# Performance work log

Hardware: AMD Instinct MI355X
Metric: run time of the kernel (lower is better)

Reference implementation:

```python
import jax, jax.numpy as jnp
import numpy as np

N = 100000      # n_nodes
E = 1600000     # n_edges (avg degree 16)
IN, HID, OUT = 128, 128, 64
P = 0.5         # dropout prob


def setup_inputs() -> dict:
    key = jax.random.key(0)
    k = jax.random.split(key, 6)
    x = jax.random.normal(k[0], (N, IN), dtype=jnp.float32)
    edge_index = jax.random.randint(k[1], (2, E), 0, N, dtype=jnp.int32)
    W1 = jax.random.normal(k[2], (IN, HID), dtype=jnp.float32) / np.sqrt(IN)
    b1 = jnp.zeros((HID,), dtype=jnp.float32)
    W2 = jax.random.normal(k[3], (HID, OUT), dtype=jnp.float32) / np.sqrt(HID)
    b2 = jnp.zeros((OUT,), dtype=jnp.float32)
    return {"x": x, "edge_index": edge_index, "W1": W1, "b1": b1, "W2": W2, "b2": b2}


def gcn_conv(x, W, b, src, dst, num_nodes):
    """PyG GCNConv: add self-loops, symmetric D^-1/2 A D^-1/2 normalization,
    linear transform then scatter-add aggregation at destination nodes."""
    loop = jnp.arange(num_nodes, dtype=src.dtype)
    s = jnp.concatenate([src, loop])  # [E+N]
    d = jnp.concatenate([dst, loop])
    deg = jax.ops.segment_sum(jnp.ones_like(d, dtype=x.dtype), d, num_segments=num_nodes)
    dinv = jnp.where(deg > 0, jax.lax.rsqrt(jnp.maximum(deg, 1e-12)), 0.0)
    norm = dinv[s] * dinv[d]                     # [E+N]
    h = x @ W                                    # [N, F_out] (transform first: cheaper)
    msg = h[s] * norm[:, None]                   # gather + scale
    out = jax.ops.segment_sum(msg, d, num_segments=num_nodes)  # scatter-add
    return out + b


def reference(x, edge_index, W1, b1, W2, b2):
    src, dst = edge_index[0], edge_index[1]
    h = jax.nn.relu(gcn_conv(x, W1, b1, src, dst, N))
    # F.dropout(training=True) with a fixed key for determinism
    keep = jax.random.bernoulli(jax.random.key(42), 1.0 - P, h.shape)
    h = jnp.where(keep, h / (1.0 - P), 0.0)
    return gcn_conv(h, W2, b2, src, dst, N)
```

## Files before the change

### kernel.cpp

```cpp
#include <hip/hip_runtime.h>


constexpr int NN    = 100000;
constexpr int NE    = 1600000;
constexpr int SCAN_CHUNK = 2048;
constexpr int NSCAN = (NN + SCAN_CHUNK - 1) / SCAN_CHUNK;

typedef __attribute__((ext_vector_type(8))) short short8v;
typedef __attribute__((ext_vector_type(4))) float f32x4;

__device__ __forceinline__ float bf2f(unsigned short u) {
  return __uint_as_float(((unsigned)u) << 16);
}
__device__ __forceinline__ unsigned short f2bf(float f) {
  unsigned x = __float_as_uint(f);
  return (unsigned short)((x + 0x7fffu + ((x >> 16) & 1u)) >> 16);
}
__device__ __forceinline__ float lo16(unsigned p) { return bf2f((unsigned short)(p & 0xffffu)); }
__device__ __forceinline__ float hi16(unsigned p) { return bf2f((unsigned short)(p >> 16)); }

__device__ __forceinline__ unsigned tf_rotl(unsigned x, int r) {
  return (x << r) | (x >> (32 - r));
}

__device__ __forceinline__ void threefry2x32_0_42(unsigned in0, unsigned in1,
                                                  unsigned& o0, unsigned& o1) {
  const unsigned K0 = 0u, K1 = 42u;
  const unsigned K2 = 0x1BD11BDAu ^ K0 ^ K1;
  unsigned x0 = in0 + K0, x1 = in1 + K1;
#define TFR(r) { x0 += x1; x1 = tf_rotl(x1, r); x1 ^= x0; }
  TFR(13) TFR(15) TFR(26) TFR(6)
  x0 += K1; x1 += K2 + 1u;
  TFR(17) TFR(29) TFR(16) TFR(24)
  x0 += K2; x1 += K0 + 2u;
  TFR(13) TFR(15) TFR(26) TFR(6)
  x0 += K0; x1 += K1 + 3u;
  TFR(17) TFR(29) TFR(16) TFR(24)
  x0 += K1; x1 += K2 + 4u;
  TFR(13) TFR(15) TFR(26) TFR(6)
  x0 += K2; x1 += K0 + 5u;
#undef TFR
  o0 = x0; o1 = x1;
}

__device__ __forceinline__ bool dropout_keep(unsigned i) {
  unsigned a, b; threefry2x32_0_42(0u, i, a, b);
  return ((a ^ b) >> 31) == 0u;
}


__global__ __launch_bounds__(256) void hist_kernel(const int* __restrict__ dst,
                                                   int* __restrict__ cnt) {
  int e = blockIdx.x * 256 + threadIdx.x;
  if (e < NE) atomicAdd(&cnt[dst[e]], 1);
}

__global__ __launch_bounds__(256) void scan1_kernel(const int* __restrict__ cnt,
                                                    int* __restrict__ off,
                                                    int* __restrict__ blksum,
                                                    float* __restrict__ dinv) {
  __shared__ int tsum[256];
  const int base = blockIdx.x * SCAN_CHUNK + threadIdx.x * 8;
  int v[8]; int s = 0;
#pragma unroll
  for (int j = 0; j < 8; j++) {
    int idx = base + j;
    v[j] = (idx < NN) ? cnt[idx] : 0;
    s += v[j];
    if (idx < NN) dinv[idx] = rsqrtf((float)v[j] + 1.0f);
  }
  tsum[threadIdx.x] = s;
  __syncthreads();
  for (int d = 1; d < 256; d <<= 1) {
    int t = (threadIdx.x >= d) ? tsum[threadIdx.x - d] : 0;
    __syncthreads();
    tsum[threadIdx.x] += t;
    __syncthreads();
  }
  int run = tsum[threadIdx.x] - s;
  if (threadIdx.x == 255) blksum[blockIdx.x] = tsum[255];
#pragma unroll
  for (int j = 0; j < 8; j++) {
    int idx = base + j;
    if (idx < NN) { off[idx] = run; run += v[j]; }
  }
}

__global__ void scan2_kernel(int* __restrict__ blksum, int* __restrict__ off) {
  if (threadIdx.x == 0) {
    int run = 0;
    for (int i = 0; i < NSCAN; i++) { int t = blksum[i]; blksum[i] = run; run += t; }
    off[NN] = NE;
  }
}

__global__ __launch_bounds__(256) void scan3_kernel(int* __restrict__ off,
                                                    const int* __restrict__ blksum) {
  const int base = blockIdx.x * SCAN_CHUNK + threadIdx.x * 8;
  const int add = blksum[blockIdx.x];
#pragma unroll
  for (int j = 0; j < 8; j++) {
    int idx = base + j;
    if (idx < NN) off[idx] += add;
  }
}

__global__ __launch_bounds__(256) void permute_kernel(const int* __restrict__ src,
                                                      const int* __restrict__ dst,
                                                      int* __restrict__ cur,
                                                      int* __restrict__ srcs) {
  int e = blockIdx.x * 256 + threadIdx.x;
  if (e >= NE) return;
  int p = atomicAdd(&cur[dst[e]], 1);
  srcs[p] = src[e];
}


template <int C, bool BF16_IN>
__global__ __launch_bounds__(256) void gemm_mfma_kernel(const void* __restrict__ Xv,
                                                        const float* __restrict__ W,
                                                        unsigned short* __restrict__ H,
                                                        int nrows) {
  constexpr int STR = 136;
  __shared__ unsigned short Xs[64 * STR];
  __shared__ unsigned short Wt[C * STR];
  const int row0 = blockIdx.x * 64;
  const int nr = min(64, nrows - row0);
  const int tid = threadIdx.x;

  for (int t = tid; t < C * 64; t += 256) {
    int n = t % C, kk = t / C;
    unsigned pk = ((unsigned)f2bf(W[(2 * kk + 1) * C + n]) << 16) | f2bf(W[(2 * kk) * C + n]);
    *(unsigned*)&Wt[n * STR + 2 * kk] = pk;
  }
  if (BF16_IN) {
    const unsigned* X = (const unsigned*)Xv + (size_t)row0 * 64;
    for (int t = tid; t < 64 * 64; t += 256) {
      int r = t >> 6, kp = t & 63;
      unsigned p = (r < nr) ? X[r * 64 + kp] : 0u;
      *(unsigned*)&Xs[r * STR + 2 * kp] = p;
    }
  } else {
    const float* X = (const float*)Xv + (size_t)row0 * 128;
    for (int t = tid; t < 64 * 64; t += 256) {
      int r = t >> 6, kp = t & 63;
      unsigned p = 0u;
      if (r < nr) {
        float2 v = *(const float2*)&X[r * 128 + 2 * kp];
        p = ((unsigned)f2bf(v.y) << 16) | f2bf(v.x);
      }
      *(unsigned*)&Xs[r * STR + 2 * kp] = p;
    }
  }
  __syncthreads();

  const int w  = tid >> 6;
  const int l  = tid & 63;
  const int lr = l & 15;
  const int lk = l >> 4;
  constexpr int NT = C / 16;

  f32x4 acc[NT];
#pragma unroll
  for (int nt = 0; nt < NT; nt++) acc[nt] = (f32x4){0.f, 0.f, 0.f, 0.f};

  short8v afr[4];
  const int arow = w * 16 + lr;
#pragma unroll
  for (int ks = 0; ks < 4; ks++)
    afr[ks] = *(const short8v*)&Xs[arow * STR + ks * 32 + lk * 8];

#pragma unroll
  for (int nt = 0; nt < NT; nt++) {
    const int ncol = nt * 16 + lr;
#pragma unroll
    for (int ks = 0; ks < 4; ks++) {
      short8v bfr = *(const short8v*)&Wt[ncol * STR + ks * 32 + lk * 8];
      acc[nt] = __builtin_amdgcn_mfma_f32_16x16x32_bf16(afr[ks], bfr, acc[nt], 0, 0, 0);
    }
  }

#pragma unroll
  for (int nt = 0; nt < NT; nt++) {
#pragma unroll
    for (int r = 0; r < 4; r++) {
      int row = w * 16 + lk * 4 + r;
      if (row < nr) H[(size_t)(row0 + row) * C + nt * 16 + lr] = f2bf(acc[nt][r]);
    }
  }
}


__global__ __launch_bounds__(256) void gather1_kernel(const int* __restrict__ off,
                                                      const int* __restrict__ srcs,
                                                      const unsigned* __restrict__ hb,
                                                      const float* __restrict__ dinv,
                                                      const float* __restrict__ b1,
                                                      unsigned* __restrict__ hd) {
  int nid = blockIdx.x * 4 + (threadIdx.x >> 6);
  if (nid >= NN) return;
  int c = threadIdx.x & 63;
  float di = dinv[nid];
  unsigned hp = hb[(size_t)nid * 64 + c];
  float a0 = lo16(hp) * di * di;
  float a1 = hi16(hp) * di * di;
  int beg = off[nid], end = off[nid + 1];
  int e = beg;
  for (; e + 8 <= end; e += 8) {
    int s[8]; float w[8]; unsigned p[8];
#pragma unroll
    for (int j = 0; j < 8; j++) s[j] = srcs[e + j];
#pragma unroll
    for (int j = 0; j < 8; j++) w[j] = dinv[s[j]] * di;
#pragma unroll
    for (int j = 0; j < 8; j++) p[j] = hb[(size_t)s[j] * 64 + c];
#pragma unroll
    for (int j = 0; j < 8; j++) {
      a0 = fmaf(lo16(p[j]), w[j], a0);
      a1 = fmaf(hi16(p[j]), w[j], a1);
    }
  }
  for (; e < end; e++) {
    int s = srcs[e];
    float w = dinv[s] * di;
    unsigned p = hb[(size_t)s * 64 + c];
    a0 = fmaf(lo16(p), w, a0);
    a1 = fmaf(hi16(p), w, a1);
  }
  a0 += b1[2 * c];
  a1 += b1[2 * c + 1];
  a0 = fmaxf(a0, 0.f);
  a1 = fmaxf(a1, 0.f);
  unsigned i0 = (unsigned)nid * 128u + 2u * (unsigned)c;
  a0 = dropout_keep(i0)      ? 2.f * a0 : 0.f;
  a1 = dropout_keep(i0 + 1u) ? 2.f * a1 : 0.f;
  hd[(size_t)nid * 64 + c] = ((unsigned)f2bf(a1) << 16) | f2bf(a0);
}


__global__ __launch_bounds__(256) void gather2_kernel(const int* __restrict__ off,
                                                      const int* __restrict__ srcs,
                                                      const unsigned short* __restrict__ h2b,
                                                      const float* __restrict__ dinv,
                                                      const float* __restrict__ b2,
                                                      float* __restrict__ out) {
  int nid = blockIdx.x * 4 + (threadIdx.x >> 6);
  if (nid >= NN) return;
  int c = threadIdx.x & 63;
  float di = dinv[nid];
  float acc = bf2f(h2b[(size_t)nid * 64 + c]) * di * di;
  int beg = off[nid], end = off[nid + 1];
  int e = beg;
  for (; e + 8 <= end; e += 8) {
    int s[8]; float w[8]; float v[8];
#pragma unroll
    for (int j = 0; j < 8; j++) s[j] = srcs[e + j];
#pragma unroll
    for (int j = 0; j < 8; j++) w[j] = dinv[s[j]] * di;
#pragma unroll
    for (int j = 0; j < 8; j++) v[j] = bf2f(h2b[(size_t)s[j] * 64 + c]);
#pragma unroll
    for (int j = 0; j < 8; j++) acc = fmaf(v[j], w[j], acc);
  }
  for (; e < end; e++) {
    int s = srcs[e];
    acc = fmaf(bf2f(h2b[(size_t)s * 64 + c]), dinv[s] * di, acc);
  }
  out[(size_t)nid * 64 + c] = acc + b2[c];
}


extern "C" void kernel_launch(void* const* d_in, const int* in_sizes, int n_in,
                              void* d_out, int out_size, void* d_ws, size_t ws_size,
                              hipStream_t stream) {
  const float* x  = (const float*)d_in[0];
  const int*   ei = (const int*)d_in[1];
  const float* W1 = (const float*)d_in[2];
  const float* b1 = (const float*)d_in[3];
  const float* W2 = (const float*)d_in[4];
  const float* b2 = (const float*)d_in[5];
  float* out = (float*)d_out;

  const int* src = ei;
  const int* dst = ei + NE;

  char* p = (char*)d_ws;
  auto take = [&](size_t bytes) { char* q = p; p += (bytes + 15) & ~size_t(15); return q; };
  int*      cnt    = (int*)take(sizeof(int) * NN);
  int*      cur    = (int*)take(sizeof(int) * NN);
  int*      off    = (int*)take(sizeof(int) * (NN + 1));
  int*      blksum = (int*)take(sizeof(int) * NSCAN);
  float*    dinv   = (float*)take(sizeof(float) * NN);
  int*      srcs   = (int*)take(sizeof(int) * NE);
  unsigned* hb     = (unsigned*)take(sizeof(unsigned) * (size_t)NN * 64);
  unsigned* hd     = (unsigned*)take(sizeof(unsigned) * (size_t)NN * 64);
  unsigned* h2b    = (unsigned*)take(sizeof(unsigned) * (size_t)NN * 32);

  hipMemsetAsync(cnt, 0, sizeof(int) * NN, stream);
  hist_kernel<<<(NE + 255) / 256, 256, 0, stream>>>(dst, cnt);
  scan1_kernel<<<NSCAN, 256, 0, stream>>>(cnt, off, blksum, dinv);
  scan2_kernel<<<1, 64, 0, stream>>>(blksum, off);
  scan3_kernel<<<NSCAN, 256, 0, stream>>>(off, blksum);
  hipMemcpyAsync(cur, off, sizeof(int) * NN, hipMemcpyDeviceToDevice, stream);
  permute_kernel<<<(NE + 255) / 256, 256, 0, stream>>>(src, dst, cur, srcs);

  gemm_mfma_kernel<128, false><<<(NN + 63) / 64, 256, 0, stream>>>(
      x, W1, (unsigned short*)hb, NN);
  gather1_kernel<<<(NN + 3) / 4, 256, 0, stream>>>(off, srcs, hb, dinv, b1, hd);

  gemm_mfma_kernel<64, true><<<(NN + 63) / 64, 256, 0, stream>>>(
      hd, W2, (unsigned short*)h2b, NN);
  gather2_kernel<<<(NN + 3) / 4, 256, 0, stream>>>(
      off, srcs, (const unsigned short*)h2b, dinv, b2, out);
}
```

Baseline: 513.9 us.

## Build CSR with two-level bucket sort instead of per-node atomics

```diff
diff --git a/kernel.cpp b/kernel.cpp
--- a/kernel.cpp
+++ b/kernel.cpp
@@ -1,10 +1,9 @@
 #include <hip/hip_runtime.h>
 
 
-constexpr int NN    = 100000;
-constexpr int NE    = 1600000;
-constexpr int SCAN_CHUNK = 2048;
-constexpr int NSCAN = (NN + SCAN_CHUNK - 1) / SCAN_CHUNK;
+constexpr int NN = 100000;
+constexpr int NE = 1600000;
+constexpr int NB = (NN + 127) / 128;
 
 typedef __attribute__((ext_vector_type(8))) short short8v;
 typedef __attribute__((ext_vector_type(4))) float f32x4;
@@ -49,70 +48,91 @@
 }
 
 
-__global__ __launch_bounds__(256) void hist_kernel(const int* __restrict__ dst,
-                                                   int* __restrict__ cnt) {
-  int e = blockIdx.x * 256 + threadIdx.x;
-  if (e < NE) atomicAdd(&cnt[dst[e]], 1);
-}
-
-__global__ __launch_bounds__(256) void scan1_kernel(const int* __restrict__ cnt,
-                                                    int* __restrict__ off,
-                                                    int* __restrict__ blksum,
-                                                    float* __restrict__ dinv) {
-  __shared__ int tsum[256];
-  const int base = blockIdx.x * SCAN_CHUNK + threadIdx.x * 8;
-  int v[8]; int s = 0;
-#pragma unroll
-  for (int j = 0; j < 8; j++) {
-    int idx = base + j;
-    v[j] = (idx < NN) ? cnt[idx] : 0;
-    s += v[j];
-    if (idx < NN) dinv[idx] = rsqrtf((float)v[j] + 1.0f);
-  }
-  tsum[threadIdx.x] = s;
-  __syncthreads();
-  for (int d = 1; d < 256; d <<= 1) {
-    int t = (threadIdx.x >= d) ? tsum[threadIdx.x - d] : 0;
+__global__ __launch_bounds__(256) void histB_kernel(const int* __restrict__ dst,
+                                                    int* __restrict__ bcnt) {
+  __shared__ int h[NB];
+  for (int i = threadIdx.x; i < NB; i += 256) h[i] = 0;
+  __syncthreads();
+  for (int e = blockIdx.x * 256 + threadIdx.x; e < NE; e += gridDim.x * 256)
+    atomicAdd(&h[dst[e] >> 7], 1);
+  __syncthreads();
+  for (int i = threadIdx.x; i < NB; i += 256)
+    if (h[i]) atomicAdd(&bcnt[i], h[i]);
+}
+
+__global__ __launch_bounds__(1024) void scanB_kernel(const int* __restrict__ bcnt,
+                                                     int* __restrict__ bbase,
+                                                     int* __restrict__ bcur,
+                                                     int* __restrict__ off) {
+  __shared__ int s[1024];
+  int t = threadIdx.x;
+  s[t] = (t < NB) ? bcnt[t] : 0;
+  __syncthreads();
+  for (int d = 1; d < 1024; d <<= 1) {
+    int v = (t >= d) ? s[t - d] : 0;
     __syncthreads();
-    tsum[threadIdx.x] += t;
+    s[t] += v;
     __syncthreads();
   }
-  int run = tsum[threadIdx.x] - s;
-  if (threadIdx.x == 255) blksum[blockIdx.x] = tsum[255];
-#pragma unroll
-  for (int j = 0; j < 8; j++) {
-    int idx = base + j;
-    if (idx < NN) { off[idx] = run; run += v[j]; }
-  }
-}
-
-__global__ void scan2_kernel(int* __restrict__ blksum, int* __restrict__ off) {
-  if (threadIdx.x == 0) {
-    int run = 0;
-    for (int i = 0; i < NSCAN; i++) { int t = blksum[i]; blksum[i] = run; run += t; }
-    off[NN] = NE;
-  }
-}
-
-__global__ __launch_bounds__(256) void scan3_kernel(int* __restrict__ off,
-                                                    const int* __restrict__ blksum) {
-  const int base = blockIdx.x * SCAN_CHUNK + threadIdx.x * 8;
-  const int add = blksum[blockIdx.x];
-#pragma unroll
-  for (int j = 0; j < 8; j++) {
-    int idx = base + j;
-    if (idx < NN) off[idx] += add;
-  }
-}
-
-__global__ __launch_bounds__(256) void permute_kernel(const int* __restrict__ src,
-                                                      const int* __restrict__ dst,
-                                                      int* __restrict__ cur,
-                                                      int* __restrict__ srcs) {
+  if (t < NB) {
+    int base = (t == 0) ? 0 : s[t - 1];
+    bbase[t] = base;
+    bcur[t] = base;
+  }
+  if (t == 0) { bbase[NB] = NE; off[NN] = NE; }
+}
+
+__global__ __launch_bounds__(256) void scatB_kernel(const int* __restrict__ src,
+                                                    const int* __restrict__ dst,
+                                                    int* __restrict__ bcur,
+                                                    unsigned* __restrict__ pairs) {
   int e = blockIdx.x * 256 + threadIdx.x;
   if (e >= NE) return;
-  int p = atomicAdd(&cur[dst[e]], 1);
-  srcs[p] = src[e];
+  int d = dst[e];
+  int p = atomicAdd(&bcur[d >> 7], 1);
+  pairs[p] = (unsigned)src[e] | ((unsigned)(d & 127) << 17);
+}
+
+__global__ __launch_bounds__(256) void sortC_kernel(const int* __restrict__ bbase,
+                                                    const unsigned* __restrict__ pairs,
+                                                    int* __restrict__ off,
+                                                    float* __restrict__ dinv,
+                                                    int* __restrict__ srcs) {
+  __shared__ int hcnt[128];
+  __shared__ int hoff[128];
+  const int b = blockIdx.x;
+  const int beg = bbase[b], end = bbase[b + 1];
+  const int t = threadIdx.x;
+  if (t < 128) hcnt[t] = 0;
+  __syncthreads();
+  for (int i = beg + t; i < end; i += 256)
+    atomicAdd(&hcnt[pairs[i] >> 17], 1);
+  __syncthreads();
+  if (t < 128) hoff[t] = hcnt[t];
+  __syncthreads();
+  for (int d = 1; d < 128; d <<= 1) {
+    int v = (t < 128 && t >= d) ? hoff[t - d] : 0;
+    __syncthreads();
+    if (t < 128) hoff[t] += v;
+    __syncthreads();
+  }
+  if (t < 128) {
+    int cnt = hcnt[t];
+    int excl = hoff[t] - cnt;
+    int n = b * 128 + t;
+    if (n < NN) {
+      off[n] = beg + excl;
+      dinv[n] = rsqrtf((float)cnt + 1.0f);
+    }
+  }
+  __syncthreads();
+  if (t < 128) hcnt[t] = hoff[t] - hcnt[t];
+  __syncthreads();
+  for (int i = beg + t; i < end; i += 256) {
+    unsigned w = pairs[i];
+    int pos = atomicAdd(&hcnt[w >> 17], 1);
+    srcs[beg + pos] = (int)(w & 0x1FFFFu);
+  }
 }
 
 
@@ -286,23 +306,22 @@
 
   char* p = (char*)d_ws;
   auto take = [&](size_t bytes) { char* q = p; p += (bytes + 15) & ~size_t(15); return q; };
-  int*      cnt    = (int*)take(sizeof(int) * NN);
-  int*      cur    = (int*)take(sizeof(int) * NN);
-  int*      off    = (int*)take(sizeof(int) * (NN + 1));
-  int*      blksum = (int*)take(sizeof(int) * NSCAN);
-  float*    dinv   = (float*)take(sizeof(float) * NN);
-  int*      srcs   = (int*)take(sizeof(int) * NE);
-  unsigned* hb     = (unsigned*)take(sizeof(unsigned) * (size_t)NN * 64);
-  unsigned* hd     = (unsigned*)take(sizeof(unsigned) * (size_t)NN * 64);
-  unsigned* h2b    = (unsigned*)take(sizeof(unsigned) * (size_t)NN * 32);
-
-  hipMemsetAsync(cnt, 0, sizeof(int) * NN, stream);
-  hist_kernel<<<(NE + 255) / 256, 256, 0, stream>>>(dst, cnt);
-  scan1_kernel<<<NSCAN, 256, 0, stream>>>(cnt, off, blksum, dinv);
-  scan2_kernel<<<1, 64, 0, stream>>>(blksum, off);
-  scan3_kernel<<<NSCAN, 256, 0, stream>>>(off, blksum);
-  hipMemcpyAsync(cur, off, sizeof(int) * NN, hipMemcpyDeviceToDevice, stream);
-  permute_kernel<<<(NE + 255) / 256, 256, 0, stream>>>(src, dst, cur, srcs);
+  int*      bcnt  = (int*)take(sizeof(int) * NB);
+  int*      bbase = (int*)take(sizeof(int) * (NB + 1));
+  int*      bcur  = (int*)take(sizeof(int) * NB);
+  unsigned* pairs = (unsigned*)take(sizeof(unsigned) * NE);
+  int*      off   = (int*)take(sizeof(int) * (NN + 1));
+  float*    dinv  = (float*)take(sizeof(float) * NN);
+  int*      srcs  = (int*)take(sizeof(int) * NE);
+  unsigned* hb    = (unsigned*)take(sizeof(unsigned) * (size_t)NN * 64);
+  unsigned* hd    = (unsigned*)take(sizeof(unsigned) * (size_t)NN * 64);
+  unsigned* h2b   = (unsigned*)take(sizeof(unsigned) * (size_t)NN * 32);
+
+  hipMemsetAsync(bcnt, 0, sizeof(int) * NB, stream);
+  histB_kernel<<<256, 256, 0, stream>>>(dst, bcnt);
+  scanB_kernel<<<1, 1024, 0, stream>>>(bcnt, bbase, bcur, off);
+  scatB_kernel<<<(NE + 255) / 256, 256, 0, stream>>>(src, dst, bcur, pairs);
+  sortC_kernel<<<NB, 256, 0, stream>>>(bbase, pairs, off, dinv, srcs);
 
   gemm_mfma_kernel<128, false><<<(NN + 63) / 64, 256, 0, stream>>>(
       x, W1, (unsigned short*)hb, NN);
```

Result: slower. 726.7 us (+41.4%).
